# Optimization experiments

Measured on AMD Instinct MI355X. Metric: run time of the kernel, lower is better.

The kernel has to match this reference:

```python
import jax, jax.numpy as jnp
import numpy as np
from jax import lax

P = 4
PSIZE = P * P
ITERS = 3
EPS = 1e-8
LAMBDA = 1e-3  # inverse-temperature used by the EM routing sigmoid (yl-1993 style)
LN2PI_HALF = 0.5 * float(np.log(2.0 * np.pi))


def extract_patches(x, K, stride, pad):
    """x: (b,h,w,c) -> (b,oh,ow,K*K,c) sliding-window patches."""
    if pad:
        x = jnp.pad(x, ((0, 0), (pad, pad), (pad, pad), (0, 0)))
    b, h, w, c = x.shape
    oh = (h - K) // stride + 1
    ow = (w - K) // stride + 1
    slices = []
    for ki in range(K):
        for kj in range(K):
            slices.append(x[:, ki:ki + stride * (oh - 1) + 1:stride,
                             kj:kj + stride * (ow - 1) + 1:stride, :])
    return jnp.stack(slices, axis=3)  # (b,oh,ow,K*K,c)


def em_routing(v, a_in, beta_u, beta_a, iters=ITERS):
    """EM routing (Hinton et al. 2018).
    v: (n, Bin, Cout, PSIZE) votes, a_in: (n, Bin, 1) input activations.
    Returns mu: (n, Cout, PSIZE), a_out: (n, Cout).
    """
    n, Bin, Cout, psize = v.shape
    r = jnp.full((n, Bin, Cout), 1.0 / Cout, dtype=v.dtype)
    mu = None
    a_out = None
    for it in range(iters):
        # ---- M step ----
        r_w = r * a_in                                    # (n,Bin,Cout)
        r_sum = r_w.sum(axis=1, keepdims=True)            # (n,1,Cout)
        coeff = (r_w / (r_sum + EPS))[..., None]          # (n,Bin,Cout,1)
        mu = jnp.sum(coeff * v, axis=1, keepdims=True)    # (n,1,Cout,psize)
        sigma_sq = jnp.sum(coeff * (v - mu) ** 2, axis=1, keepdims=True) + EPS
        cost_h = (beta_u[None, None, :, None] + 0.5 * jnp.log(sigma_sq)) * r_sum[..., None]
        a_out = jax.nn.sigmoid(LAMBDA * (beta_a[None, None, :] - cost_h.sum(axis=3)))  # (n,1,Cout)
        # ---- E step ----
        if it < iters - 1:
            ln_p = -(v - mu) ** 2 / (2.0 * sigma_sq) - 0.5 * jnp.log(sigma_sq) - LN2PI_HALF
            ln_ap = ln_p.sum(axis=3) + jnp.log(EPS + a_out)  # (n,Bin,Cout)
            r = jax.nn.softmax(ln_ap, axis=2)
    return mu[:, 0], a_out[:, 0]


def depthwise_caps(pose, a, W, bu, ba, K, stride):
    """DepthWiseConvCaps: each capsule type routes its own KxK spatial patch to one
    output capsule of the same type. W: (K*K, B, P, P)."""
    b = pose.shape[0]
    Bc = a.shape[-1]
    pad = K // 2
    pp = extract_patches(pose, K, stride, pad)  # (b,oh,ow,KK,B*PSIZE)
    ap = extract_patches(a, K, stride, pad)     # (b,oh,ow,KK,B)
    oh, ow = pp.shape[1], pp.shape[2]
    pm = pp.reshape(b, oh, ow, K * K, Bc, P, P)
    v = jnp.einsum('bhwkcij,kcjl->bhwkcil', pm, W)            # (b,oh,ow,KK,B,P,P)
    v = v.transpose(0, 1, 2, 4, 3, 5, 6).reshape(b * oh * ow * Bc, K * K, 1, PSIZE)
    a_in = ap.transpose(0, 1, 2, 4, 3).reshape(b * oh * ow * Bc, K * K, 1)
    mu, a_out = em_routing(v, a_in, bu, ba)
    return mu.reshape(b, oh, ow, Bc * PSIZE), a_out.reshape(b, oh, ow, Bc)


def conv_caps_1x1(pose, a, W, bu, ba):
    """ConvCaps with K=1, stride=1: per-position routing Bin -> Cout. W: (Bin,Cout,P,P)."""
    b, h, w, _ = pose.shape
    Bc, Cc = W.shape[0], W.shape[1]
    pm = pose.reshape(b * h * w, Bc, P, P)
    v = jnp.einsum('nbij,bcjl->nbcil', pm, W).reshape(b * h * w, Bc, Cc, PSIZE)
    a_in = a.reshape(b * h * w, Bc)[..., None]
    mu, a_out = em_routing(v, a_in, bu, ba)
    return mu.reshape(b, h, w, Cc * PSIZE), a_out.reshape(b, h, w, Cc)


def class_caps(pose, a, W, bu, ba):
    """Class ConvCaps: w_shared across positions + coordinate addition. W: (D,E,P,P)."""
    b, h, w, _ = pose.shape
    D, E = W.shape[0], W.shape[1]
    pm = pose.reshape(b, h, w, D, P, P)
    v = jnp.einsum('bhwdij,dejl->bhwdeil', pm, W).reshape(b, h, w, D, E, PSIZE)
    # coordinate addition on the first two vote components
    coord = jnp.zeros((h, w, PSIZE), v.dtype)
    coord = coord.at[:, :, 0].add(jnp.arange(h, dtype=v.dtype)[:, None] / h)
    coord = coord.at[:, :, 1].add(jnp.arange(w, dtype=v.dtype)[None, :] / w)
    v = v + coord[None, :, :, None, None, :]
    v = v.reshape(b, h * w * D, E, PSIZE)
    a_in = a.reshape(b, h * w * D, 1)
    mu, a_out = em_routing(v, a_in, bu, ba)
    return mu, a_out  # (b,E,PSIZE), (b,E)


def _forward(x, conv1_w, conv1_b, prim_pose_w, prim_pose_b, prim_a_w, prim_a_b,
             dw1_w, dw1_bu, dw1_ba, cc1_w, cc1_bu, cc1_ba,
             dw2_w, dw2_bu, dw2_ba, cc2_w, cc2_bu, cc2_ba,
             cls_w, cls_bu, cls_ba):
    # conv stem: k5 s2 valid
    y = lax.conv_general_dilated(x, conv1_w, (2, 2), 'VALID',
                                 dimension_numbers=('NHWC', 'HWIO', 'NHWC'))
    y = jax.nn.relu(y + conv1_b)
    # primary caps: 1x1 convs for pose and activation
    pose = jnp.einsum('bhwc,cd->bhwd', y, prim_pose_w) + prim_pose_b   # (b,h,w,B*PSIZE)
    a = jax.nn.sigmoid(jnp.einsum('bhwc,cd->bhwd', y, prim_a_w) + prim_a_b)  # (b,h,w,B)
    pose, a = depthwise_caps(pose, a, dw1_w, dw1_bu, dw1_ba, K=7, stride=2)
    pose, a = conv_caps_1x1(pose, a, cc1_w, cc1_bu, cc1_ba)
    pose, a = depthwise_caps(pose, a, dw2_w, dw2_bu, dw2_ba, K=5, stride=2)
    pose, a = conv_caps_1x1(pose, a, cc2_w, cc2_bu, cc2_ba)
    pose_cls, a_cls = class_caps(pose, a, cls_w, cls_bu, cls_ba)
    return a_cls  # (b, E)


def setup_inputs() -> dict:
    key = jax.random.key(0)
    ks = jax.random.split(key, 10)
    f32 = jnp.float32
    d = {}
    d['x'] = jax.random.normal(ks[0], (32, 64, 64, 1), f32)
    d['conv1_w'] = jax.random.normal(ks[1], (5, 5, 1, 64), f32) * 0.1
    d['conv1_b'] = jnp.zeros((64,), f32)
    d['prim_pose_w'] = jax.random.normal(ks[2], (64, 128), f32) * 0.1
    d['prim_pose_b'] = jnp.zeros((128,), f32)
    d['prim_a_w'] = jax.random.normal(ks[3], (64, 8), f32) * 0.1
    d['prim_a_b'] = jnp.zeros((8,), f32)
    d['dw1_w'] = jax.random.normal(ks[4], (49, 8, 4, 4), f32) * 0.25
    d['dw1_bu'] = jnp.zeros((1,), f32)
    d['dw1_ba'] = jnp.zeros((1,), f32)
    d['cc1_w'] = jax.random.normal(ks[5], (8, 16, 4, 4), f32) * 0.25
    d['cc1_bu'] = jnp.zeros((16,), f32)
    d['cc1_ba'] = jnp.zeros((16,), f32)
    d['dw2_w'] = jax.random.normal(ks[6], (25, 16, 4, 4), f32) * 0.25
    d['dw2_bu'] = jnp.zeros((1,), f32)
    d['dw2_ba'] = jnp.zeros((1,), f32)
    d['cc2_w'] = jax.random.normal(ks[7], (16, 16, 4, 4), f32) * 0.25
    d['cc2_bu'] = jnp.zeros((16,), f32)
    d['cc2_ba'] = jnp.zeros((16,), f32)
    d['cls_w'] = jax.random.normal(ks[8], (16, 10, 4, 4), f32) * 0.25
    d['cls_bu'] = jnp.zeros((10,), f32)
    d['cls_ba'] = jnp.zeros((10,), f32)
    return d


def reference(x, conv1_w, conv1_b, prim_pose_w, prim_pose_b, prim_a_w, prim_a_b,
              dw1_w, dw1_bu, dw1_ba, cc1_w, cc1_bu, cc1_ba,
              dw2_w, dw2_bu, dw2_ba, cc2_w, cc2_bu, cc2_ba,
              cls_w, cls_bu, cls_ba):
    return _forward(x, conv1_w, conv1_b, prim_pose_w, prim_pose_b, prim_a_w, prim_a_b,
                    dw1_w, dw1_bu, dw1_ba, cc1_w, cc1_bu, cc1_ba,
                    dw2_w, dw2_bu, dw2_ba, cc2_w, cc2_bu, cc2_ba,
                    cls_w, cls_bu, cls_ba)
```

## Files before the change

### kernel.cpp

```cpp
#include <hip/hip_runtime.h>
#include <hip/hip_bf16.h>

#define EPS 1e-8f
#define LAMBDA 1e-3f
#define LN2PI_HALF 0.9189385332046727f

__device__ __forceinline__ float sigmoidf(float x) { return 1.f / (1.f + __expf(-x)); }

__global__ __launch_bounds__(256) void stem_primary_kernel(
    const float* __restrict__ x, const float* __restrict__ w,
    const float* __restrict__ bias,
    const float* __restrict__ wp, const float* __restrict__ bp,
    const float* __restrict__ wa, const float* __restrict__ ba,
    float* __restrict__ pose, float* __restrict__ a) {
  __shared__ __align__(16) float wp_s[64][128];
  __shared__ __align__(16) float wc_s[25][64];
  __shared__ __align__(16) float wa_s[64][8];
  __shared__ __align__(16) float bias_s[64];
  __shared__ __align__(16) float bp_s[128];
  __shared__ float ba_s[8];
  __shared__ float xs[5][63];
  __shared__ __align__(16) float ys_u[2][15][68];

  int t = threadIdx.x;
  int oi = blockIdx.x % 30;
  int b  = blockIdx.x / 30;

  for (int q = t; q < 2048; q += 256) ((float4*)wp_s)[q] = ((const float4*)wp)[q];
  for (int q = t; q < 400;  q += 256) ((float4*)wc_s)[q] = ((const float4*)w)[q];
  for (int q = t; q < 128;  q += 256) ((float4*)wa_s)[q] = ((const float4*)wa)[q];
  if (t < 64) bias_s[t] = bias[t];
  if (t < 128) bp_s[t] = bp[t];
  if (t < 8) ba_s[t] = ba[t];
  for (int q = t; q < 315; q += 256) {
    int ki = q / 63, col = q % 63;
    xs[ki][col] = x[(b * 64 + 2 * oi + ki) * 64 + col];
  }
  __syncthreads();

  for (int q = t; q < 480; q += 256) {
    int pos = q >> 4, c4 = (q & 15) << 2;
    float4 s4 = *(const float4*)&bias_s[c4];
#pragma unroll
    for (int ki = 0; ki < 5; ++ki)
#pragma unroll
      for (int kj = 0; kj < 5; ++kj) {
        float xv = xs[ki][2 * pos + kj];
        const float4 wv = *(const float4*)&wc_s[ki * 5 + kj][c4];
        s4.x += xv * wv.x;
        s4.y += xv * wv.y;
        s4.z += xv * wv.z;
        s4.w += xv * wv.w;
      }
    s4.x = fmaxf(s4.x, 0.f);
    s4.y = fmaxf(s4.y, 0.f);
    s4.z = fmaxf(s4.z, 0.f);
    s4.w = fmaxf(s4.w, 0.f);
    *(float4*)&ys_u[pos & 1][pos >> 1][c4] = s4;
  }
  __syncthreads();

  int w_ = t >> 7, d = t & 127;
  float acc[15];
#pragma unroll
  for (int j = 0; j < 15; ++j) acc[j] = bp_s[d];
#pragma unroll 4
  for (int c4 = 0; c4 < 64; c4 += 4) {
    float w0 = wp_s[c4 + 0][d];
    float w1 = wp_s[c4 + 1][d];
    float w2 = wp_s[c4 + 2][d];
    float w3 = wp_s[c4 + 3][d];
#pragma unroll
    for (int j = 0; j < 15; ++j) {
      const float4 yv = *(const float4*)&ys_u[w_][j][c4];
      acc[j] += yv.x * w0 + yv.y * w1 + yv.z * w2 + yv.w * w3;
    }
  }
  size_t rowb = (size_t)(b * 30 + oi) * 30;
#pragma unroll
  for (int j = 0; j < 15; ++j)
    pose[(rowb + w_ + 2 * j) * 128 + d] = acc[j];

  if (t < 240) {
    int pos = t >> 3, jj = t & 7;
    float s = ba_s[jj];
#pragma unroll 8
    for (int c = 0; c < 64; ++c) s += ys_u[pos & 1][pos >> 1][c] * wa_s[c][jj];
    a[(rowb + pos) * 8 + jj] = sigmoidf(s);
  }
}

template <int K, int BC, int HIN, int WIN, int HOUT, int WOUT, int OIG, int NG>
__global__ __launch_bounds__(256) void dw_caps_kernel(
    const float* __restrict__ pose_in, const float* __restrict__ a_in,
    const float* __restrict__ Wt,
    const float* __restrict__ bu_p, const float* __restrict__ ba_p,
    float* __restrict__ pose_out, float* __restrict__ a_out) {
  constexpr int PAD = K / 2;
  constexpr int RA = (2 * (OIG - 1) + K < HIN) ? (2 * (OIG - 1) + K) : HIN;
  constexpr int TOT = OIG * WOUT * 16;
  constexpr int KM = (TOT + 255) / 256;
  __shared__ __align__(16) float tp[RA * WIN * 20];
  __shared__ float ta[RA * WIN];
  __shared__ __align__(16) float wt[K * K * 16];

  int t = threadIdx.x;
  int g = (NG > 1) ? (blockIdx.x % NG) : 0;
  int c = (blockIdx.x / NG) % BC;
  int b = blockIdx.x / (NG * BC);
  int oi_lo = g * OIG;
  int rlo = max(0, 2 * oi_lo - PAD);
  int rhi = min(HIN, 2 * (oi_lo + OIG - 1) - PAD + K);
  int nrows = rhi - rlo;

  for (int q = t; q < K * K * 16; q += 256) {
    int tap = q >> 4, lj = q & 15, l = lj >> 2, j = lj & 3;
    wt[tap * 16 + lj] = Wt[((size_t)tap * BC + c) * 16 + j * 4 + l];
  }
  for (int q = t; q < nrows * WIN; q += 256) {
    int row = q / WIN, col = q % WIN;
    ta[q] = a_in[((size_t)((b * HIN + rlo + row) * WIN + col)) * BC + c];
  }
  for (int q = t; q < nrows * WIN * 4; q += 256) {
    int quad = q & 3, pc = q >> 2;
    int row = pc / WIN, col = pc % WIN;
    const float4 src = *(const float4*)(pose_in +
        (((size_t)((b * HIN + rlo + row) * WIN + col)) * BC + c) * 16 + quad * 4);
    *(float4*)(tp + (row * WIN + col) * 20 + quad * 4) = src;
  }
  __syncthreads();

  const int p = t & 15;
  const int ip = p >> 2, l = p & 3;
  const float* wtl = wt + l * 4;

  int ih0[KM], iw0[KM];
  float rsum[KM], acc[KM], acc2[KM];
#pragma unroll
  for (int k = 0; k < KM; ++k) {
    int s = t + k * 256;
    int pr = s >> 4;
    int oj = pr % WOUT;
    int oi = oi_lo + pr / WOUT;
    ih0[k] = 2 * oi - PAD;
    iw0[k] = 2 * oj - PAD;
    rsum[k] = 0.f;
    acc[k] = 0.f;
    acc2[k] = 0.f;
  }

#pragma unroll 1
  for (int ki = 0; ki < K; ++ki) {
    int rb[KM];
    bool vk[KM];
#pragma unroll
    for (int k = 0; k < KM; ++k) {
      int ih = ih0[k] + ki;
      vk[k] = (t + k * 256 < TOT) && (ih >= 0) && (ih < HIN);
      rb[k] = (ih - rlo) * WIN;
    }
#pragma unroll
    for (int kj = 0; kj < K; ++kj) {
      const float4 wr = *(const float4*)(wtl + (ki * K + kj) * 16);
#pragma unroll
      for (int k = 0; k < KM; ++k) {
        if (!vk[k]) continue;
        int iw = iw0[k] + kj;
        if (iw < 0 || iw >= WIN) continue;
        int idx = rb[k] + iw;
        float ak = ta[idx];
        const float4 pm = *(const float4*)(tp + idx * 20 + ip * 4);
        float v = pm.x * wr.x + pm.y * wr.y + pm.z * wr.z + pm.w * wr.w;
        rsum[k] += ak;
        float av = ak * v;
        acc[k] += av;
        acc2[k] += av * v;
      }
    }
  }

#pragma unroll 1
  for (int k = 0; k < KM; ++k) {
    int s = t + k * 256;
    if (s >= TOT) break;
    int pr = s >> 4;
    int oj = pr % WOUT;
    int oi = oi_lo + pr / WOUT;
    float inv = 1.f / (rsum[k] + EPS);
    float mu = acc[k] * inv;
    float S = rsum[k] * inv;
    float sg = acc2[k] * inv - mu * mu * (2.f - S);
    sg = fmaxf(sg, 0.f) + EPS;
    float hl = 0.5f * __logf(sg);
    float ls = hl;
    ls += __shfl_xor(ls, 1, 64);
    ls += __shfl_xor(ls, 2, 64);
    ls += __shfl_xor(ls, 4, 64);
    ls += __shfl_xor(ls, 8, 64);

    size_t obase = ((size_t)(b * HOUT + oi) * WOUT + oj) * BC + c;
    pose_out[obase * 16 + p] = mu;
    if (p == 0) {
      float cost = rsum[k] * (16.f * bu_p[0] + ls);
      a_out[obase] = sigmoidf(LAMBDA * (ba_p[0] - cost));
    }
  }
}

template <int BIN>
__global__ __launch_bounds__(256) void cc_em_kernel(
    const float* __restrict__ pose_in, const float* __restrict__ a_arr,
    const float* __restrict__ Wt,
    const float* __restrict__ bu_p, const float* __restrict__ ba_p,
    float* __restrict__ pose_out, float* __restrict__ a_out) {
  constexpr int COUT = 16;
  __shared__ float wt_s[BIN * COUT * 20];
  int t = threadIdx.x;
  for (int idx = t; idx < BIN * COUT * 16; idx += 256) {
    int lk = idx & 15, l = lk >> 2, k = lk & 3;
    int bc = idx >> 4;
    wt_s[bc * 20 + l * 4 + k] = Wt[bc * 16 + k * 4 + l];
  }
  __syncthreads();

  int wave = t >> 6, lane = t & 63;
  int n = blockIdx.x * 4 + wave;
  int c = lane >> 2;
  int q = lane & 3;

  float ain[BIN], rw[BIN];
  float4 pmq[BIN];
#pragma unroll
  for (int b = 0; b < BIN; ++b) {
    ain[b] = a_arr[(size_t)n * BIN + b];
    rw[b] = (1.f / 16.f) * ain[b];
    pmq[b] = *(const float4*)(pose_in + (size_t)n * BIN * 16 + b * 16 + q * 4);
  }
  float bu = bu_p[c], ba = ba_p[c];

  float v[BIN][4];
#pragma unroll
  for (int b = 0; b < BIN; ++b) {
    const float* wr = wt_s + (b * 16 + c) * 20;
#pragma unroll
    for (int l = 0; l < 4; ++l) {
      const float4 w4 = *(const float4*)(wr + l * 4);
      v[b][l] = pmq[b].x * w4.x + pmq[b].y * w4.y + pmq[b].z * w4.z + pmq[b].w * w4.w;
    }
  }

  float mu[4], inv2[4], lsum = 0.f, ao = 0.f;
#pragma unroll 1
  for (int it = 0; it < 3; ++it) {
    float sA = 0.f, sV[4] = {0, 0, 0, 0}, sV2[4] = {0, 0, 0, 0};
#pragma unroll
    for (int b = 0; b < BIN; ++b) {
      sA += rw[b];
#pragma unroll
      for (int l = 0; l < 4; ++l) {
        float rv = rw[b] * v[b][l];
        sV[l] += rv;
        sV2[l] += rv * v[b][l];
      }
    }
    float inv = 1.f / (sA + EPS);
    float S = sA * inv;
    lsum = 0.f;
#pragma unroll
    for (int l = 0; l < 4; ++l) {
      mu[l] = sV[l] * inv;
      float sg = sV2[l] * inv - mu[l] * mu[l] * (2.f - S) + EPS;
      sg = fmaxf(sg, EPS);
      inv2[l] = 0.5f / sg;
      lsum += 0.5f * __logf(sg);
    }
    lsum += __shfl_xor(lsum, 1, 64);
    lsum += __shfl_xor(lsum, 2, 64);
    float cost = sA * (16.f * bu + lsum);
    ao = sigmoidf(LAMBDA * (ba - cost));

    if (it < 2) {
      float term[BIN];
#pragma unroll
      for (int b = 0; b < BIN; ++b) {
        float s = 0.f;
#pragma unroll
        for (int l = 0; l < 4; ++l) {
          float d = v[b][l] - mu[l];
          s += d * d * inv2[l];
        }
        term[b] = s;
      }
#pragma unroll
      for (int b = 0; b < BIN; ++b) {
        term[b] += __shfl_xor(term[b], 1, 64);
        term[b] += __shfl_xor(term[b], 2, 64);
      }
      float basec = __logf(EPS + ao) - lsum - 16.f * LN2PI_HALF;
      float lnap[BIN], Z[BIN];
#pragma unroll
      for (int b = 0; b < BIN; ++b) lnap[b] = basec - term[b];
      float mx[BIN];
#pragma unroll
      for (int b = 0; b < BIN; ++b) mx[b] = lnap[b];
#pragma unroll
      for (int m = 4; m < 64; m <<= 1)
#pragma unroll
        for (int b = 0; b < BIN; ++b) mx[b] = fmaxf(mx[b], __shfl_xor(mx[b], m, 64));
#pragma unroll
      for (int b = 0; b < BIN; ++b) { lnap[b] = __expf(lnap[b] - mx[b]); Z[b] = lnap[b]; }
#pragma unroll
      for (int m = 4; m < 64; m <<= 1)
#pragma unroll
        for (int b = 0; b < BIN; ++b) Z[b] += __shfl_xor(Z[b], m, 64);
#pragma unroll
      for (int b = 0; b < BIN; ++b) rw[b] = lnap[b] / Z[b] * ain[b];
    }
  }
  float4 om = make_float4(mu[0], mu[1], mu[2], mu[3]);
  *(float4*)(pose_out + (size_t)n * 256 + c * 16 + q * 4) = om;
  if (q == 0) a_out[(size_t)n * COUT + c] = ao;
}

__global__ __launch_bounds__(256) void cls_m_kernel(
    const float* __restrict__ pose5, const float* __restrict__ a5,
    const float* __restrict__ X, const float* __restrict__ W,
    const float* __restrict__ bu_p, const float* __restrict__ ba_p,
    float* __restrict__ mu_g, float* __restrict__ inv2_g,
    float* __restrict__ base_g, float* __restrict__ out,
    int first, int last) {
  int blk = blockIdx.x;
  int c = blk % 10, b = blk / 10;
  int t = threadIdx.x;
  int lane = t & 63, wv = t >> 6;
  const float* pg = pose5 + (size_t)b * 16384;
  __shared__ float w_s[16][16];
  {
    int d = t & 15, jj = t >> 4;
    w_s[jj][d] = W[(d * 10 + c) * 16 + jj];
  }
  __syncthreads();
  const int d = t & 15;
  float wf[16];
#pragma unroll
  for (int jj = 0; jj < 16; ++jj) wf[jj] = w_s[jj][d];

  float sA = 0.f, sV[16], sV2[16];
#pragma unroll
  for (int p = 0; p < 16; ++p) { sV[p] = 0.f; sV2[p] = 0.f; }
#pragma unroll 1
  for (int rep = 0; rep < 4; ++rep) {
    int bi = rep * 256 + t;
    int pos = bi >> 4;
    float rw = first ? 0.1f * a5[(size_t)b * 1024 + bi]
                     : X[(size_t)blk * 1024 + bi];
    float ci = (float)(pos >> 3) * 0.125f;
    float cj = (float)(pos & 7) * 0.125f;
    const float* pp = pg + pos * 256 + d * 16;
    float pmr[16];
#pragma unroll
    for (int q = 0; q < 16; ++q) pmr[q] = pp[q];
    sA += rw;
#pragma unroll
    for (int p = 0; p < 16; ++p) {
      int ip = p >> 2, l = p & 3;
      float v = pmr[ip * 4 + 0] * wf[0 * 4 + l] + pmr[ip * 4 + 1] * wf[1 * 4 + l]
              + pmr[ip * 4 + 2] * wf[2 * 4 + l] + pmr[ip * 4 + 3] * wf[3 * 4 + l];
      if (p == 0) v += ci;
      else if (p == 1) v += cj;
      float rv = rw * v;
      sV[p] += rv;
      sV2[p] += rv * v;
    }
  }
#pragma unroll
  for (int off = 1; off < 64; off <<= 1) {
    sA += __shfl_xor(sA, off, 64);
#pragma unroll
    for (int p = 0; p < 16; ++p) {
      sV[p]  += __shfl_xor(sV[p],  off, 64);
      sV2[p] += __shfl_xor(sV2[p], off, 64);
    }
  }
  __shared__ float red[4][36];
  if (lane == 0) {
    red[wv][0] = sA;
#pragma unroll
    for (int p = 0; p < 16; ++p) { red[wv][1 + p] = sV[p]; red[wv][17 + p] = sV2[p]; }
  }
  __syncthreads();
  if (t < 16) {
    int p = t;
    float sAf  = red[0][0] + red[1][0] + red[2][0] + red[3][0];
    float sVf  = red[0][1+p] + red[1][1+p] + red[2][1+p] + red[3][1+p];
    float sV2f = red[0][17+p] + red[1][17+p] + red[2][17+p] + red[3][17+p];
    float inv = 1.f / (sAf + EPS);
    float S = sAf * inv;
    float mu = sVf * inv;
    float sg = sV2f * inv - mu * mu * (2.f - S) + EPS;
    sg = fmaxf(sg, EPS);
    mu_g[blk * 16 + p] = mu;
    inv2_g[blk * 16 + p] = 0.5f / sg;
    float hl = 0.5f * __logf(sg);
    float lsum = hl;
    lsum += __shfl_xor(lsum, 1, 64);
    lsum += __shfl_xor(lsum, 2, 64);
    lsum += __shfl_xor(lsum, 4, 64);
    lsum += __shfl_xor(lsum, 8, 64);
    if (p == 0) {
      float cost = sAf * (16.f * bu_p[c] + lsum);
      float ao = sigmoidf(LAMBDA * (ba_p[c] - cost));
      base_g[blk] = __logf(EPS + ao) - lsum - 16.f * LN2PI_HALF;
      if (last) out[blk] = ao;
    }
  }
}

__global__ __launch_bounds__(512) void cls_e_kernel(
    const float* __restrict__ pose5, const float* __restrict__ a5,
    const float* __restrict__ W,
    const float* __restrict__ mu_g, const float* __restrict__ inv2_g,
    const float* __restrict__ base_g, float* __restrict__ X) {
  int b = blockIdx.x >> 1;
  int t = threadIdx.x;
  int bi = ((blockIdx.x & 1) << 9) + t;
  const float* pg = pose5 + (size_t)b * 16384;
  __shared__ float w2[10][16][16];
  __shared__ float mu_s[160];
  __shared__ float inv2_s[160];
  __shared__ float base_s[10];
  for (int q = t; q < 2560; q += 512) {
    int dd = q & 15, jj = (q >> 4) & 15, c = q >> 8;
    w2[c][jj][dd] = W[(dd * 10 + c) * 16 + jj];
  }
  if (t < 160) { mu_s[t] = mu_g[b * 160 + t]; inv2_s[t] = inv2_g[b * 160 + t]; }
  if (t >= 160 && t < 170) base_s[t - 160] = base_g[b * 10 + (t - 160)];
  __syncthreads();

  int pos = bi >> 4, d2 = bi & 15;
  float ci = (float)(pos >> 3) * 0.125f;
  float cj = (float)(pos & 7) * 0.125f;
  const float* pp = pg + pos * 256 + d2 * 16;
  float pmr[16];
#pragma unroll
  for (int q = 0; q < 16; ++q) pmr[q] = pp[q];
  float lnap[10];
#pragma unroll 1
  for (int c = 0; c < 10; ++c) {
    float wf[16];
#pragma unroll
    for (int jj = 0; jj < 16; ++jj) wf[jj] = w2[c][jj][d2];
    float s = base_s[c];
#pragma unroll
    for (int p = 0; p < 16; ++p) {
      int ip = p >> 2, l = p & 3;
      float v = pmr[ip * 4 + 0] * wf[0 * 4 + l] + pmr[ip * 4 + 1] * wf[1 * 4 + l]
              + pmr[ip * 4 + 2] * wf[2 * 4 + l] + pmr[ip * 4 + 3] * wf[3 * 4 + l];
      if (p == 0) v += ci;
      else if (p == 1) v += cj;
      float dd = v - mu_s[c * 16 + p];
      s -= dd * dd * inv2_s[c * 16 + p];
    }
    lnap[c] = s;
  }
  float m = -1e30f;
#pragma unroll
  for (int c = 0; c < 10; ++c) m = fmaxf(m, lnap[c]);
  float Z = 0.f;
  float ex[10];
#pragma unroll
  for (int c = 0; c < 10; ++c) { ex[c] = __expf(lnap[c] - m); Z += ex[c]; }
  float invZ = a5[(size_t)b * 1024 + bi] / Z;
#pragma unroll
  for (int c = 0; c < 10; ++c) X[((size_t)(b * 10 + c)) * 1024 + bi] = ex[c] * invZ;
}

extern "C" void kernel_launch(void* const* d_in, const int* in_sizes, int n_in,
                              void* d_out, int out_size, void* d_ws, size_t ws_size,
                              hipStream_t stream) {
  const float* x       = (const float*)d_in[0];
  const float* conv1_w = (const float*)d_in[1];
  const float* conv1_b = (const float*)d_in[2];
  const float* pp_w    = (const float*)d_in[3];
  const float* pp_b    = (const float*)d_in[4];
  const float* pa_w    = (const float*)d_in[5];
  const float* pa_b    = (const float*)d_in[6];
  const float* dw1_w   = (const float*)d_in[7];
  const float* dw1_bu  = (const float*)d_in[8];
  const float* dw1_ba  = (const float*)d_in[9];
  const float* cc1_w   = (const float*)d_in[10];
  const float* cc1_bu  = (const float*)d_in[11];
  const float* cc1_ba  = (const float*)d_in[12];
  const float* dw2_w   = (const float*)d_in[13];
  const float* dw2_bu  = (const float*)d_in[14];
  const float* dw2_ba  = (const float*)d_in[15];
  const float* cc2_w   = (const float*)d_in[16];
  const float* cc2_bu  = (const float*)d_in[17];
  const float* cc2_ba  = (const float*)d_in[18];
  const float* cls_w   = (const float*)d_in[19];
  const float* cls_bu  = (const float*)d_in[20];
  const float* cls_ba  = (const float*)d_in[21];
  float* out = (float*)d_out;

  float* ws = (float*)d_ws;
  float* pose1 = ws;
  float* a1    = ws + 3686400;
  float* pose2 = ws + 3916800;
  float* a2    = ws + 4838400;
  float* pose3 = ws;
  float* a3    = ws + 1843200;
  float* pose4 = ws + 1958400;
  float* a4    = ws + 2482688;
  float* pose5 = ws + 2515456;
  float* a5    = ws + 3039744;
  float* Xbuf  = ws + 3072512;
  float* mu_g  = ws + 3400192;
  float* inv2_g= ws + 3405312;
  float* base_g= ws + 3410432;

  stem_primary_kernel<<<960, 256, 0, stream>>>(x, conv1_w, conv1_b,
                                               pp_w, pp_b, pa_w, pa_b, pose1, a1);
  dw_caps_kernel<7, 8, 30, 30, 15, 15, 5, 3><<<768, 256, 0, stream>>>(
      pose1, a1, dw1_w, dw1_bu, dw1_ba, pose2, a2);
  cc_em_kernel<8><<<1800, 256, 0, stream>>>(pose2, a2, cc1_w, cc1_bu, cc1_ba, pose3, a3);
  dw_caps_kernel<5, 16, 15, 15, 8, 8, 8, 1><<<512, 256, 0, stream>>>(
      pose3, a3, dw2_w, dw2_bu, dw2_ba, pose4, a4);
  cc_em_kernel<16><<<512, 256, 0, stream>>>(pose4, a4, cc2_w, cc2_bu, cc2_ba, pose5, a5);
  cls_m_kernel<<<320, 256, 0, stream>>>(pose5, a5, Xbuf, cls_w, cls_bu, cls_ba,
                                        mu_g, inv2_g, base_g, out, 1, 0);
  cls_e_kernel<<<64, 512, 0, stream>>>(pose5, a5, cls_w, mu_g, inv2_g, base_g, Xbuf);
  cls_m_kernel<<<320, 256, 0, stream>>>(pose5, a5, Xbuf, cls_w, cls_bu, cls_ba,
                                        mu_g, inv2_g, base_g, out, 0, 0);
  cls_e_kernel<<<64, 512, 0, stream>>>(pose5, a5, cls_w, mu_g, inv2_g, base_g, Xbuf);
  cls_m_kernel<<<320, 256, 0, stream>>>(pose5, a5, Xbuf, cls_w, cls_bu, cls_ba,
                                        mu_g, inv2_g, base_g, out, 0, 1);
}
```

Before: 262.1 us.

## Split 16-input capsule EM routing across four waves per position

Replaces the second convolutional-capsule EM kernel with a version where each block handles one output position and its four wavefronts each own four of the sixteen input capsules. Partial M-step sums are combined through double-buffered shared memory with one barrier per iteration, and sigma is computed from moments instead of a second pass. The aim is to cut per-thread register and serial work and expose more parallelism (2048 blocks instead of 512), at the cost of extra block barriers, shared-memory traffic and redundant per-wave M-step math.

```diff
diff --git a/kernel.cpp b/kernel.cpp
--- a/kernel.cpp
+++ b/kernel.cpp
@@ -320,6 +320,124 @@
   float4 om = make_float4(mu[0], mu[1], mu[2], mu[3]);
   *(float4*)(pose_out + (size_t)n * 256 + c * 16 + q * 4) = om;
   if (q == 0) a_out[(size_t)n * COUT + c] = ao;
+}
+
+__global__ __launch_bounds__(256) void cc_em_coop16_kernel(
+    const float* __restrict__ pose_in, const float* __restrict__ a_arr,
+    const float* __restrict__ Wt,
+    const float* __restrict__ bu_p, const float* __restrict__ ba_p,
+    float* __restrict__ pose_out, float* __restrict__ a_out) {
+  __shared__ float red_s[2][4][64 * 9];
+  int t = threadIdx.x;
+  int w = t >> 6, lane = t & 63;
+  int c = lane >> 2, q = lane & 3;
+  int n = blockIdx.x;
+
+  float ain[4], rw[4], v[4][4];
+  const float* pbase = pose_in + (size_t)n * 256;
+#pragma unroll
+  for (int i = 0; i < 4; ++i) {
+    int b = w * 4 + i;
+    ain[i] = a_arr[(size_t)n * 16 + b];
+    rw[i] = (1.f / 16.f) * ain[i];
+    const float4 pm = *(const float4*)(pbase + b * 16 + q * 4);
+    const float* wr = Wt + (b * 16 + c) * 16;
+    const float4 r0 = *(const float4*)(wr + 0);
+    const float4 r1 = *(const float4*)(wr + 4);
+    const float4 r2 = *(const float4*)(wr + 8);
+    const float4 r3 = *(const float4*)(wr + 12);
+    v[i][0] = pm.x * r0.x + pm.y * r1.x + pm.z * r2.x + pm.w * r3.x;
+    v[i][1] = pm.x * r0.y + pm.y * r1.y + pm.z * r2.y + pm.w * r3.y;
+    v[i][2] = pm.x * r0.z + pm.y * r1.z + pm.z * r2.z + pm.w * r3.z;
+    v[i][3] = pm.x * r0.w + pm.y * r1.w + pm.z * r2.w + pm.w * r3.w;
+  }
+  float bu = bu_p[c], ba = ba_p[c];
+
+  float mu[4], inv2[4], lsum = 0.f, ao = 0.f;
+#pragma unroll 1
+  for (int it = 0; it < 3; ++it) {
+    float psA = 0.f, psV[4] = {0, 0, 0, 0}, psV2[4] = {0, 0, 0, 0};
+#pragma unroll
+    for (int i = 0; i < 4; ++i) {
+      psA += rw[i];
+#pragma unroll
+      for (int l = 0; l < 4; ++l) {
+        float rv = rw[i] * v[i][l];
+        psV[l] += rv;
+        psV2[l] += rv * v[i][l];
+      }
+    }
+    {
+      float* rs = &red_s[it & 1][w][lane * 9];
+      rs[0] = psA;
+#pragma unroll
+      for (int l = 0; l < 4; ++l) { rs[1 + l] = psV[l]; rs[5 + l] = psV2[l]; }
+    }
+    __syncthreads();
+    float sA = 0.f, sV[4] = {0, 0, 0, 0}, sV2[4] = {0, 0, 0, 0};
+#pragma unroll
+    for (int w2 = 0; w2 < 4; ++w2) {
+      const float* rr = &red_s[it & 1][w2][lane * 9];
+      sA += rr[0];
+#pragma unroll
+      for (int l = 0; l < 4; ++l) { sV[l] += rr[1 + l]; sV2[l] += rr[5 + l]; }
+    }
+    float inv = 1.f / (sA + EPS);
+    float S = sA * inv;
+    lsum = 0.f;
+#pragma unroll
+    for (int l = 0; l < 4; ++l) {
+      mu[l] = sV[l] * inv;
+      float sg = sV2[l] * inv - mu[l] * mu[l] * (2.f - S) + EPS;
+      sg = fmaxf(sg, EPS);
+      inv2[l] = 0.5f / sg;
+      lsum += 0.5f * __logf(sg);
+    }
+    lsum += __shfl_xor(lsum, 1, 64);
+    lsum += __shfl_xor(lsum, 2, 64);
+    float cost = sA * (16.f * bu + lsum);
+    ao = sigmoidf(LAMBDA * (ba - cost));
+
+    if (it < 2) {
+      float term[4];
+#pragma unroll
+      for (int i = 0; i < 4; ++i) {
+        float s = 0.f;
+#pragma unroll
+        for (int l = 0; l < 4; ++l) {
+          float d = v[i][l] - mu[l];
+          s += d * d * inv2[l];
+        }
+        term[i] = s;
+      }
+#pragma unroll
+      for (int i = 0; i < 4; ++i) {
+        term[i] += __shfl_xor(term[i], 1, 64);
+        term[i] += __shfl_xor(term[i], 2, 64);
+      }
+      float basec = __logf(EPS + ao) - lsum - 16.f * LN2PI_HALF;
+      float lnap[4], mx[4], Z[4];
+#pragma unroll
+      for (int i = 0; i < 4; ++i) { lnap[i] = basec - term[i]; mx[i] = lnap[i]; }
+#pragma unroll
+      for (int m = 4; m < 64; m <<= 1)
+#pragma unroll
+        for (int i = 0; i < 4; ++i) mx[i] = fmaxf(mx[i], __shfl_xor(mx[i], m, 64));
+#pragma unroll
+      for (int i = 0; i < 4; ++i) { lnap[i] = __expf(lnap[i] - mx[i]); Z[i] = lnap[i]; }
+#pragma unroll
+      for (int m = 4; m < 64; m <<= 1)
+#pragma unroll
+        for (int i = 0; i < 4; ++i) Z[i] += __shfl_xor(Z[i], m, 64);
+#pragma unroll
+      for (int i = 0; i < 4; ++i) rw[i] = lnap[i] / Z[i] * ain[i];
+    }
+  }
+  if (w == 0) {
+    *(float4*)(pose_out + (size_t)n * 256 + c * 16 + q * 4) =
+        make_float4(mu[0], mu[1], mu[2], mu[3]);
+    if (q == 0) a_out[(size_t)n * 16 + c] = ao;
+  }
 }
 
 __global__ __launch_bounds__(256) void cls_m_kernel(
@@ -525,7 +643,8 @@
   cc_em_kernel<8><<<1800, 256, 0, stream>>>(pose2, a2, cc1_w, cc1_bu, cc1_ba, pose3, a3);
   dw_caps_kernel<5, 16, 15, 15, 8, 8, 8, 1><<<512, 256, 0, stream>>>(
       pose3, a3, dw2_w, dw2_bu, dw2_ba, pose4, a4);
-  cc_em_kernel<16><<<512, 256, 0, stream>>>(pose4, a4, cc2_w, cc2_bu, cc2_ba, pose5, a5);
+  cc_em_coop16_kernel<<<2048, 256, 0, stream>>>(pose4, a4, cc2_w, cc2_bu, cc2_ba,
+                                                pose5, a5);
   cls_m_kernel<<<320, 256, 0, stream>>>(pose5, a5, Xbuf, cls_w, cls_bu, cls_ba,
                                         mu_g, inv2_g, base_g, out, 1, 0);
   cls_e_kernel<<<64, 512, 0, stream>>>(pose5, a5, cls_w, mu_g, inv2_g, base_g, Xbuf);
```

Result: no change. 258.7 us (-1.3%).
